# Kernel tuning notes

Hardware: AMD Instinct MI355X
Metric: run time of the kernel (lower is better)

The kernel has to match this reference:

```python
import jax, jax.numpy as jnp
import numpy as np

GROUP_SIZE = 128
N_BITS = 4
QMAX = 2 ** N_BITS - 1
NUM_EXPERTS = 8
HIDDEN = 2048
INTER = 768
NUM_ROT = 4
T_TOKENS = 4096
TOP_K = 2


def _make_pairs(rng, n_rot, in_feat):
    # intra-group permutation per rotation (valid disjoint Givens pairs)
    n_groups = in_feat // GROUP_SIZE
    return np.stack([
        np.concatenate([rng.permutation(GROUP_SIZE) for _ in range(n_groups)])
        for _ in range(n_rot)
    ]).astype(np.int32)


def _round_ste(x):
    return x + jax.lax.stop_gradient(jnp.round(x) - x)


def _rotate(W, pairs, angles):
    # W: [N, in_feat]; pairs: [R, in_feat] intra-group perm; angles: [R, in_feat//2]
    in_feat = W.shape[1]
    base = (jnp.arange(in_feat) // GROUP_SIZE) * GROUP_SIZE
    for r in range(pairs.shape[0]):
        abs_idx = base + pairs[r]
        i_idx = abs_idx[0::2]
        j_idx = abs_idx[1::2]
        c = jnp.cos(angles[r])
        s = jnp.sin(angles[r])
        wi = W[:, i_idx]
        wj = W[:, j_idx]
        W = W.at[:, i_idx].set(c * wi - s * wj).at[:, j_idx].set(s * wi + c * wj)
    return W


def _fake_quant(W):
    # groupwise asymmetric min-max fake quantization with STE rounding
    shape = W.shape
    wg = W.reshape(-1, GROUP_SIZE)
    wmax = wg.max(axis=-1, keepdims=True)
    wmin = wg.min(axis=-1, keepdims=True)
    scale = jnp.clip(wmax - wmin, 1e-5, None) / QMAX
    zero = jnp.round(-wmin / scale)
    q = jnp.clip(_round_ste(wg / scale) + zero, 0.0, float(QMAX))
    return ((q - zero) * scale).reshape(shape)


def _pseudo_quantize(W3, pairs, angles, ch_scales):
    # scale -> rotate -> fake-quant -> inverse rotate (reversed order, -angles) -> unscale
    E, O, In = W3.shape
    W = W3.reshape(-1, In) * ch_scales
    W = _rotate(W, pairs, angles)
    W = _fake_quant(W)
    W = _rotate(W, pairs[::-1], -angles[::-1])
    return (W / ch_scales).reshape(E, O, In)


def setup_inputs() -> dict:
    key = jax.random.key(0)
    ks = jax.random.split(key, 8)
    rng = np.random.default_rng(0)
    hidden_states = jax.random.normal(ks[0], (T_TOKENS, HIDDEN), jnp.float32)
    top_k_index = jax.random.randint(ks[1], (T_TOKENS, TOP_K), 0, NUM_EXPERTS, jnp.int32)
    logits = jax.random.normal(ks[2], (T_TOKENS, TOP_K), jnp.float32)
    top_k_weights = jax.nn.softmax(logits, axis=-1)
    gate_up_weight = jax.random.normal(ks[3], (NUM_EXPERTS, 2 * INTER, HIDDEN), jnp.float32) * 0.02
    down_weight = jax.random.normal(ks[4], (NUM_EXPERTS, HIDDEN, INTER), jnp.float32) * 0.02
    gate_up_pairs = jnp.asarray(_make_pairs(rng, NUM_ROT, HIDDEN))
    down_pairs = jnp.asarray(_make_pairs(rng, NUM_ROT, INTER))
    gate_up_angles = jax.random.normal(ks[5], (NUM_ROT, HIDDEN // 2), jnp.float32) * 0.1
    down_angles = jax.random.normal(ks[6], (NUM_ROT, INTER // 2), jnp.float32) * 0.1
    k7, k8 = jax.random.split(ks[7])
    gate_up_channel_scales = jax.random.uniform(k7, (1, HIDDEN), jnp.float32, 0.5, 1.5)
    down_channel_scales = jax.random.uniform(k8, (1, INTER), jnp.float32, 0.5, 1.5)
    return {
        "hidden_states": hidden_states,
        "top_k_index": top_k_index,
        "top_k_weights": top_k_weights,
        "gate_up_weight": gate_up_weight,
        "down_weight": down_weight,
        "gate_up_pairs": gate_up_pairs,
        "gate_up_angles": gate_up_angles,
        "down_pairs": down_pairs,
        "down_angles": down_angles,
        "gate_up_channel_scales": gate_up_channel_scales,
        "down_channel_scales": down_channel_scales,
    }


def reference(hidden_states, top_k_index, top_k_weights, gate_up_weight, down_weight,
              gate_up_pairs, gate_up_angles, down_pairs, down_angles,
              gate_up_channel_scales, down_channel_scales):
    # dequantize expert weights
    gup = _pseudo_quantize(gate_up_weight, gate_up_pairs, gate_up_angles, gate_up_channel_scales)  # [E,2I,H]
    dwn = _pseudo_quantize(down_weight, down_pairs, down_angles, down_channel_scales)              # [E,H,I]
    T = hidden_states.shape[0]
    E = gup.shape[0]
    # dense dispatch: all experts for all tokens (E small), combined by routing weights
    h = jnp.einsum('th,eoh->teo', hidden_states, gup)          # [T,E,2I]
    gate, up = jnp.split(h, 2, axis=-1)
    inter = jax.nn.silu(gate) * up                              # [T,E,I]
    y = jnp.einsum('tei,ehi->teh', inter, dwn)                  # [T,E,H]
    combine = jnp.zeros((T, E), hidden_states.dtype)
    combine = combine.at[jnp.arange(T)[:, None], top_k_index].add(top_k_weights)
    return jnp.einsum('teh,te->th', y, combine)
```

## Files before the change

kernel.cpp:

```cpp
#include <hip/hip_runtime.h>

#define T_TOKENS 4096
#define HIDDEN   2048
#define INTERM   768
#define NE       8
#define NPAIR    8192
#define NROT     4
#define MAXT     72

typedef __bf16 bf16x8 __attribute__((ext_vector_type(8)));
typedef float  f32x4  __attribute__((ext_vector_type(4)));

__device__ __forceinline__ unsigned short f2bf(float f) {
  unsigned u = __float_as_uint(f);
  u += 0x7fffu + ((u >> 16) & 1u);
  return (unsigned short)(u >> 16);
}

__device__ __forceinline__ void async16(const void* g, void* l) {
  __builtin_amdgcn_global_load_lds((const __attribute__((address_space(1))) void*)g,
                                   (__attribute__((address_space(3))) void*)l, 16, 0, 0);
}

__global__ void k_hist(const int* __restrict__ idx, int* __restrict__ cnt) {
  const int t = blockIdx.x * 256 + threadIdx.x;
  if (t < NPAIR) atomicAdd(&cnt[idx[t]], 1);
}

__global__ void k_scan(const int* __restrict__ cnt, int* __restrict__ off,
                       int* __restrict__ cur, int* __restrict__ tmap) {
  if (threadIdx.x == 0) {
    int a = 0, tt = 0;
    for (int e = 0; e < NE; ++e) {
      off[e] = a; cur[e] = 0;
      const int c = cnt[e];
      for (int m = 0; m < c; m += 128) tmap[tt++] = (e << 16) | (m >> 7);
      a += c;
    }
    for (; tt < MAXT; ++tt) tmap[tt] = -1;
  }
}

__global__ void k_scatter(const int* __restrict__ idx, const float* __restrict__ wts,
                          const int* __restrict__ off, int* __restrict__ cur,
                          int* __restrict__ pt, float* __restrict__ pw) {
  const int t = blockIdx.x * 256 + threadIdx.x;
  if (t < NPAIR) {
    const int e = idx[t];
    const int pos = off[e] + atomicAdd(&cur[e], 1);
    pt[pos] = t;
    pw[pos] = wts[t];
  }
}

__global__ void k_tbl(const int* __restrict__ gp, const float* __restrict__ ga,
                      const int* __restrict__ dp, const float* __restrict__ da,
                      const float* __restrict__ gch, const float* __restrict__ dch,
                      float4* __restrict__ tg, float4* __restrict__ td,
                      float* __restrict__ grch, float* __restrict__ drch) {
  const int t = blockIdx.x * 256 + threadIdx.x;
  if (t < NROT * (HIDDEN / 2)) {
    const int r = t >> 10, s = t & 1023;
    const int grp = s >> 6;
    const int i = gp[r * HIDDEN + 2 * s], j = gp[r * HIDDEN + 2 * s + 1];
    const float a = ga[r * (HIDDEN / 2) + s];
    const float c = cosf(a), sn = sinf(a);
    tg[(grp * NROT + r) * 128 + i] = make_float4(c, -sn, __int_as_float(j), 0.f);
    tg[(grp * NROT + r) * 128 + j] = make_float4(c,  sn, __int_as_float(i), 0.f);
  }
  if (t < NROT * (INTERM / 2)) {
    const int r = t / (INTERM / 2), s = t - r * (INTERM / 2);
    const int grp = s >> 6;
    const int i = dp[r * INTERM + 2 * s], j = dp[r * INTERM + 2 * s + 1];
    const float a = da[r * (INTERM / 2) + s];
    const float c = cosf(a), sn = sinf(a);
    td[(grp * NROT + r) * 128 + i] = make_float4(c, -sn, __int_as_float(j), 0.f);
    td[(grp * NROT + r) * 128 + j] = make_float4(c,  sn, __int_as_float(i), 0.f);
  }
  if (t < HIDDEN) grch[t] = 1.0f / gch[t];
  if (t < INTERM) drch[t] = 1.0f / dch[t];
}

#define FWD_ROT(tl, v0, v1)                                                     \
  _Pragma("unroll")                                                             \
  for (int r = 0; r < NROT; ++r) {                                              \
    const float4 e0 = tl[r * 128 + l];                                          \
    const float4 e1 = tl[r * 128 + 64 + l];                                     \
    const int p0 = __float_as_int(e0.z), p1 = __float_as_int(e1.z);             \
    const int a0 = (p0 & 63) << 2, a1 = (p1 & 63) << 2;                         \
    _Pragma("unroll")                                                           \
    for (int q = 0; q < 4; ++q) {                                               \
      const int x0 = __float_as_int(v0[q]), x1 = __float_as_int(v1[q]);         \
      const float lo0 = __int_as_float(__builtin_amdgcn_ds_bpermute(a0, x0));   \
      const float hi0 = __int_as_float(__builtin_amdgcn_ds_bpermute(a0, x1));   \
      const float lo1 = __int_as_float(__builtin_amdgcn_ds_bpermute(a1, x0));   \
      const float hi1 = __int_as_float(__builtin_amdgcn_ds_bpermute(a1, x1));   \
      const float op0 = (p0 & 64) ? hi0 : lo0;                                  \
      const float op1 = (p1 & 64) ? hi1 : lo1;                                  \
      {                                                                         \
        _Pragma("clang fp contract(off)")                                       \
        v0[q] = e0.x * v0[q] + e0.y * op0;                                      \
        v1[q] = e1.x * v1[q] + e1.y * op1;                                      \
      }                                                                         \
    }                                                                           \
  }

__global__ __launch_bounds__(256) void k_quant(
    const float* __restrict__ W, const float4* __restrict__ tbl,
    const float* __restrict__ ch, unsigned short* __restrict__ out, int In, int G) {
  __shared__ float4 tl[NROT * 128];
  const int wv = threadIdx.x >> 6, l = threadIdx.x & 63;
  const int g = blockIdx.x % G;
  const int rowblk = blockIdx.x / G;
  const int row0 = rowblk * 16 + wv * 4;
  const int colbase = g << 7;
  tl[threadIdx.x]       = tbl[(size_t)g * NROT * 128 + threadIdx.x];
  tl[256 + threadIdx.x] = tbl[(size_t)g * NROT * 128 + 256 + threadIdx.x];
  __syncthreads();
  const float c0 = ch[colbase + l], c1 = ch[colbase + 64 + l];
  float v0[4], v1[4];
#pragma unroll
  for (int q = 0; q < 4; ++q) {
#pragma clang fp contract(off)
    const float* Wr = W + (size_t)(row0 + q) * In + colbase;
    v0[q] = Wr[l] * c0;
    v1[q] = Wr[64 + l] * c1;
  }
  FWD_ROT(tl, v0, v1)
#pragma unroll
  for (int q = 0; q < 4; ++q) {
    float mn = fminf(v0[q], v1[q]), mx = fmaxf(v0[q], v1[q]);
#pragma unroll
    for (int o = 32; o > 0; o >>= 1) {
      mn = fminf(mn, __shfl_xor(mn, o));
      mx = fmaxf(mx, __shfl_xor(mx, o));
    }
    {
#pragma clang fp contract(off)
      const float scale = fmaxf(mx - mn, 1e-5f) / 15.0f;
      const float zero = rintf(-mn / scale);
      const float q0 = fminf(fmaxf(rintf(v0[q] / scale) + zero, 0.0f), 15.0f);
      const float q1 = fminf(fmaxf(rintf(v1[q] / scale) + zero, 0.0f), 15.0f);
      v0[q] = (q0 - zero) * scale;
      v1[q] = (q1 - zero) * scale;
    }
  }
#pragma unroll
  for (int q = 0; q < 4; ++q) {
    unsigned short* Or = out + (size_t)(row0 + q) * In + colbase;
    Or[l]      = f2bf(v0[q]);
    Or[64 + l] = f2bf(v1[q]);
  }
}

__global__ __launch_bounds__(256) void k_rotx(
    const float* __restrict__ X, const float* __restrict__ rch,
    const float4* __restrict__ tbl, unsigned short* __restrict__ out) {
  __shared__ float4 tl[NROT * 128];
  const int wv = threadIdx.x >> 6, l = threadIdx.x & 63;
  const int g = blockIdx.x % 16;
  const int rowblk = blockIdx.x / 16;
  const int row0 = rowblk * 16 + wv * 4;
  const int colbase = g << 7;
  tl[threadIdx.x]       = tbl[(size_t)g * NROT * 128 + threadIdx.x];
  tl[256 + threadIdx.x] = tbl[(size_t)g * NROT * 128 + 256 + threadIdx.x];
  __syncthreads();
  const float i0 = rch[colbase + l], i1 = rch[colbase + 64 + l];
  float v0[4], v1[4];
#pragma unroll
  for (int q = 0; q < 4; ++q) {
    const float* Xr = X + (size_t)(row0 + q) * HIDDEN + colbase;
    v0[q] = Xr[l] * i0;
    v1[q] = Xr[64 + l] * i1;
  }
  FWD_ROT(tl, v0, v1)
#pragma unroll
  for (int q = 0; q < 4; ++q) {
    unsigned short* Or = out + (size_t)(row0 + q) * HIDDEN + colbase;
    Or[l]      = f2bf(v0[q]);
    Or[64 + l] = f2bf(v1[q]);
  }
}

__global__ __launch_bounds__(256) void k_silu2(
    const float* __restrict__ h, const float* __restrict__ pw,
    const float* __restrict__ rch, const float4* __restrict__ tbl,
    unsigned short* __restrict__ out) {
  __shared__ float4 tl[NROT * 128];
  const int wv = threadIdx.x >> 6, l = threadIdx.x & 63;
  const int g = blockIdx.x % 6;
  const int rowblk = blockIdx.x / 6;
  const int row0 = rowblk * 16 + wv * 4;
  const int colbase = g << 7;
  tl[threadIdx.x]       = tbl[(size_t)g * NROT * 128 + threadIdx.x];
  tl[256 + threadIdx.x] = tbl[(size_t)g * NROT * 128 + 256 + threadIdx.x];
  __syncthreads();
  const float i0 = rch[colbase + l], i1 = rch[colbase + 64 + l];
  float v0[4], v1[4];
#pragma unroll
  for (int q = 0; q < 4; ++q) {
    const int row = row0 + q;
    const float wgt = pw[row];
    const float* hr = h + (size_t)row * 1536 + colbase;
    const float g0 = hr[l], g1 = hr[64 + l];
    const float u0 = hr[768 + l], u1 = hr[768 + 64 + l];
    v0[q] = g0 / (1.0f + expf(-g0)) * u0 * wgt * i0;
    v1[q] = g1 / (1.0f + expf(-g1)) * u1 * wgt * i1;
  }
  FWD_ROT(tl, v0, v1)
#pragma unroll
  for (int q = 0; q < 4; ++q) {
    unsigned short* Or = out + (size_t)(row0 + q) * INTERM + colbase;
    Or[l]      = f2bf(v0[q]);
    Or[64 + l] = f2bf(v1[q]);
  }
}

template <int MODE>
__launch_bounds__(256, 4)
__global__ void k_gemm(const unsigned short* __restrict__ A,
                       const unsigned short* __restrict__ Bw,
                       float* __restrict__ C,
                       const int* __restrict__ pt,
                       const int* __restrict__ off,
                       const int* __restrict__ cnt,
                       const int* __restrict__ tmap) {
  constexpr int K = MODE ? INTERM : HIDDEN;
  constexpr int N = MODE ? HIDDEN : 2 * INTERM;
  const int tm = tmap[blockIdx.y];
  if (tm < 0) return;
  const int e = tm >> 16;
  const int m0 = (tm & 0xffff) << 7;
  const int count = cnt[e];
  const int seg = off[e];
  const int n0 = blockIdx.x * 128;
  const unsigned short* Be = Bw + (size_t)e * N * K;

  __shared__ unsigned short As[2][128 * 32];
  __shared__ unsigned short Bs[2][128 * 32];

  const int tid = threadIdx.x;
  const int w = tid >> 6;
  const int l = tid & 63;
  const int r0 = w * 16 + (l >> 2);
  const int r1 = r0 + 64;
  const int kco = (l & 3) * 8;

  int p0 = m0 + r0; if (p0 > count - 1) p0 = count - 1;
  int p1 = m0 + r1; if (p1 > count - 1) p1 = count - 1;
  size_t arow0, arow1;
  if (MODE == 0) { arow0 = (size_t)(pt[seg + p0] >> 1); arow1 = (size_t)(pt[seg + p1] >> 1); }
  else           { arow0 = (size_t)(seg + p0); arow1 = (size_t)(seg + p1); }
  const unsigned short* pa0 = A + arow0 * K + kco;
  const unsigned short* pa1 = A + arow1 * K + kco;
  const unsigned short* pb0 = Be + (size_t)(n0 + r0) * K + kco;
  const unsigned short* pb1 = Be + (size_t)(n0 + r1) * K + kco;

  const int ko = (l >> 4) * 8;
  const int mrow = (w & 1) * 64 + (l & 15);
  const int nrow = (w >> 1) * 64 + (l & 15);

  f32x4 acc[4][4];
#pragma unroll
  for (int i = 0; i < 4; ++i)
#pragma unroll
    for (int j = 0; j < 4; ++j) acc[i][j] = (f32x4)0.0f;

  {
    async16(pa0, &As[0][w * 512]);
    async16(pa1, &As[0][(w + 4) * 512]);
    async16(pb0, &Bs[0][w * 512]);
    async16(pb1, &Bs[0][(w + 4) * 512]);
  }
  int buf = 0;
  for (int k0 = 0; k0 < K; k0 += 32, buf ^= 1) {
    __syncthreads();
    bf16x8 af[4], bfr[4];
#pragma unroll
    for (int i = 0; i < 4; ++i)
      af[i] = *(const bf16x8*)&As[buf][(mrow + i * 16) * 32 + ko];
#pragma unroll
    for (int j = 0; j < 4; ++j)
      bfr[j] = *(const bf16x8*)&Bs[buf][(nrow + j * 16) * 32 + ko];
    if (k0 + 32 < K) {
      const int kn = k0 + 32;
      async16(pa0 + kn, &As[buf ^ 1][w * 512]);
      async16(pa1 + kn, &As[buf ^ 1][(w + 4) * 512]);
      async16(pb0 + kn, &Bs[buf ^ 1][w * 512]);
      async16(pb1 + kn, &Bs[buf ^ 1][(w + 4) * 512]);
    }
#pragma unroll
    for (int i = 0; i < 4; ++i)
#pragma unroll
      for (int j = 0; j < 4; ++j)
        acc[i][j] = __builtin_amdgcn_mfma_f32_16x16x32_bf16(af[i], bfr[j], acc[i][j], 0, 0, 0);
  }

  const int mb = (w & 1) * 64 + (l >> 4) * 4;
  const int nb = n0 + (w >> 1) * 64 + (l & 15);
#pragma unroll
  for (int i = 0; i < 4; ++i) {
#pragma unroll
    for (int j = 0; j < 4; ++j) {
#pragma unroll
      for (int r = 0; r < 4; ++r) {
        const int mm = m0 + mb + i * 16 + r;
        if (mm < count) {
          const int nn = nb + j * 16;
          if (MODE == 0) {
            C[(size_t)(seg + mm) * N + nn] = acc[i][j][r];
          } else {
            C[(size_t)pt[seg + mm] * N + nn] = acc[i][j][r];
          }
        }
      }
    }
  }
}

__global__ __launch_bounds__(256) void k_combine(const float4* __restrict__ y,
                                                 float4* __restrict__ out) {
  const int t = blockIdx.x;
  const float4* y0 = y + (size_t)(2 * t) * (HIDDEN / 4);
  const float4* y1 = y + (size_t)(2 * t + 1) * (HIDDEN / 4);
  float4* o = out + (size_t)t * (HIDDEN / 4);
#pragma unroll
  for (int q = 0; q < 2; ++q) {
    const int c = threadIdx.x + q * 256;
    const float4 a = y0[c], b = y1[c];
    o[c] = make_float4(a.x + b.x, a.y + b.y, a.z + b.z, a.w + b.w);
  }
}

extern "C" void kernel_launch(void* const* d_in, const int* in_sizes, int n_in,
                              void* d_out, int out_size, void* d_ws, size_t ws_size,
                              hipStream_t stream) {
  const float* hs  = (const float*)d_in[0];
  const int*   tki = (const int*)d_in[1];
  const float* tkw = (const float*)d_in[2];
  const float* guw = (const float*)d_in[3];
  const float* dww = (const float*)d_in[4];
  const int*   gupr= (const int*)d_in[5];
  const float* gua = (const float*)d_in[6];
  const int*   dwp = (const int*)d_in[7];
  const float* dwa = (const float*)d_in[8];
  const float* gus = (const float*)d_in[9];
  const float* dwsc= (const float*)d_in[10];
  float* out = (float*)d_out;
  char* ws = (char*)d_ws;

  unsigned short* gup_bf = (unsigned short*)(ws + 0);
  unsigned short* dwn_bf = (unsigned short*)(ws + 50331648);
  unsigned short* x_bf   = (unsigned short*)(ws + 75497472);
  float*          hbuf   = (float*)(ws + 92274688);
  unsigned short* interb = (unsigned short*)(ws + 142606336);
  float*          ybuf   = (float*)(ws + 75497472);
  int*            pt     = (int*)(ws + 155189248);
  float*          pw     = (float*)(ws + 155222016);
  int*            cnt    = (int*)(ws + 155254784);
  int*            off    = cnt + 8;
  int*            cur    = cnt + 16;
  int*            tmap   = cnt + 24;
  float4*         tg     = (float4*)(ws + 155258880);
  float4*         td     = (float4*)(ws + 155389952);
  float*          grch   = (float*)(ws + 155439104);
  float*          drch   = (float*)(ws + 155447296);

  (void)hipMemsetAsync(cnt, 0, 32, stream);

  k_hist<<<32, 256, 0, stream>>>(tki, cnt);
  k_scan<<<1, 64, 0, stream>>>(cnt, off, cur, tmap);
  k_scatter<<<32, 256, 0, stream>>>(tki, tkw, off, cur, pt, pw);
  k_tbl<<<16, 256, 0, stream>>>(gupr, gua, dwp, dwa, gus, dwsc, tg, td, grch, drch);
  k_rotx<<<4096, 256, 0, stream>>>(hs, grch, tg, x_bf);
  k_quant<<<12288, 256, 0, stream>>>(guw, tg, gus, gup_bf, HIDDEN, 16);
  k_quant<<<6144, 256, 0, stream>>>(dww, td, dwsc, dwn_bf, INTERM, 6);
  k_gemm<0><<<dim3(12, MAXT), 256, 0, stream>>>(x_bf, gup_bf, hbuf, pt, off, cnt, tmap);
  k_silu2<<<3072, 256, 0, stream>>>(hbuf, pw, drch, td, interb);
  k_gemm<1><<<dim3(16, MAXT), 256, 0, stream>>>(interb, dwn_bf, ybuf, pt, off, cnt, tmap);
  k_combine<<<T_TOKENS, 256, 0, stream>>>((const float4*)ybuf, (float4*)out);
}
```

Before: 543.2 us.

## Remap GEMM blocks per XCD for L2 locality and reorder LDS loads after prefetch

```diff
diff --git a/kernel.cpp b/kernel.cpp
--- a/kernel.cpp
+++ b/kernel.cpp
@@ -28,7 +28,8 @@
 }
 
 __global__ void k_scan(const int* __restrict__ cnt, int* __restrict__ off,
-                       int* __restrict__ cur, int* __restrict__ tmap) {
+                       int* __restrict__ cur, int* __restrict__ tmap,
+                       int* __restrict__ nv) {
   if (threadIdx.x == 0) {
     int a = 0, tt = 0;
     for (int e = 0; e < NE; ++e) {
@@ -37,6 +38,7 @@
       for (int m = 0; m < c; m += 128) tmap[tt++] = (e << 16) | (m >> 7);
       a += c;
     }
+    nv[0] = tt;
     for (; tt < MAXT; ++tt) tmap[tt] = -1;
   }
 }
@@ -224,16 +226,37 @@
                        const int* __restrict__ pt,
                        const int* __restrict__ off,
                        const int* __restrict__ cnt,
-                       const int* __restrict__ tmap) {
+                       const int* __restrict__ tmap,
+                       const int* __restrict__ nv) {
   constexpr int K = MODE ? INTERM : HIDDEN;
   constexpr int N = MODE ? HIDDEN : 2 * INTERM;
-  const int tm = tmap[blockIdx.y];
+  constexpr int XW = MODE ? 16 : 12;
+
+  const int hw  = blockIdx.x + XW * blockIdx.y;
+  const int xcd = hw & 7;
+  const int pos = hw >> 3;
+  const int nvalid = nv[0];
+  const int q8 = nvalid >> 3, r8 = nvalid & 7;
+  const int rs = q8 + (xcd < r8 ? 1 : 0);
+  const int y0 = xcd * q8 + (xcd < r8 ? xcd : r8);
+  if (pos >= rs * XW) return;
+  int xg, yg;
+  if (MODE == 1) {
+    xg = pos & 15; yg = y0 + (pos >> 4);
+  } else {
+    const int cap6 = rs * 6;
+    const int half = (pos >= cap6) ? 1 : 0;
+    const int rem  = pos - half * cap6;
+    xg = half * 6 + rem % 6;
+    yg = y0 + rem / 6;
+  }
+  const int tm = tmap[yg];
   if (tm < 0) return;
   const int e = tm >> 16;
   const int m0 = (tm & 0xffff) << 7;
   const int count = cnt[e];
   const int seg = off[e];
-  const int n0 = blockIdx.x * 128;
+  const int n0 = xg * 128;
   const unsigned short* Be = Bw + (size_t)e * N * K;
 
   __shared__ unsigned short As[2][128 * 32];
@@ -275,13 +298,6 @@
   int buf = 0;
   for (int k0 = 0; k0 < K; k0 += 32, buf ^= 1) {
     __syncthreads();
-    bf16x8 af[4], bfr[4];
-#pragma unroll
-    for (int i = 0; i < 4; ++i)
-      af[i] = *(const bf16x8*)&As[buf][(mrow + i * 16) * 32 + ko];
-#pragma unroll
-    for (int j = 0; j < 4; ++j)
-      bfr[j] = *(const bf16x8*)&Bs[buf][(nrow + j * 16) * 32 + ko];
     if (k0 + 32 < K) {
       const int kn = k0 + 32;
       async16(pa0 + kn, &As[buf ^ 1][w * 512]);
@@ -289,6 +305,13 @@
       async16(pb0 + kn, &Bs[buf ^ 1][w * 512]);
       async16(pb1 + kn, &Bs[buf ^ 1][(w + 4) * 512]);
     }
+    bf16x8 af[4], bfr[4];
+#pragma unroll
+    for (int i = 0; i < 4; ++i)
+      af[i] = *(const bf16x8*)&As[buf][(mrow + i * 16) * 32 + ko];
+#pragma unroll
+    for (int j = 0; j < 4; ++j)
+      bfr[j] = *(const bf16x8*)&Bs[buf][(nrow + j * 16) * 32 + ko];
 #pragma unroll
     for (int i = 0; i < 4; ++i)
 #pragma unroll
@@ -361,6 +384,7 @@
   int*            off    = cnt + 8;
   int*            cur    = cnt + 16;
   int*            tmap   = cnt + 24;
+  int*            nv     = cnt + 120;
   float4*         tg     = (float4*)(ws + 155258880);
   float4*         td     = (float4*)(ws + 155389952);
   float*          grch   = (float*)(ws + 155439104);
@@ -369,14 +393,14 @@
   (void)hipMemsetAsync(cnt, 0, 32, stream);
 
   k_hist<<<32, 256, 0, stream>>>(tki, cnt);
-  k_scan<<<1, 64, 0, stream>>>(cnt, off, cur, tmap);
+  k_scan<<<1, 64, 0, stream>>>(cnt, off, cur, tmap, nv);
   k_scatter<<<32, 256, 0, stream>>>(tki, tkw, off, cur, pt, pw);
   k_tbl<<<16, 256, 0, stream>>>(gupr, gua, dwp, dwa, gus, dwsc, tg, td, grch, drch);
   k_rotx<<<4096, 256, 0, stream>>>(hs, grch, tg, x_bf);
   k_quant<<<12288, 256, 0, stream>>>(guw, tg, gus, gup_bf, HIDDEN, 16);
   k_quant<<<6144, 256, 0, stream>>>(dww, td, dwsc, dwn_bf, INTERM, 6);
-  k_gemm<0><<<dim3(12, MAXT), 256, 0, stream>>>(x_bf, gup_bf, hbuf, pt, off, cnt, tmap);
+  k_gemm<0><<<dim3(12, MAXT), 256, 0, stream>>>(x_bf, gup_bf, hbuf, pt, off, cnt, tmap, nv);
   k_silu2<<<3072, 256, 0, stream>>>(hbuf, pw, drch, td, interb);
-  k_gemm<1><<<dim3(16, MAXT), 256, 0, stream>>>(interb, dwn_bf, ybuf, pt, off, cnt, tmap);
+  k_gemm<1><<<dim3(16, MAXT), 256, 0, stream>>>(interb, dwn_bf, ybuf, pt, off, cnt, tmap, nv);
   k_combine<<<T_TOKENS, 256, 0, stream>>>((const float4*)ybuf, (float4*)out);
 }
```

Measured after the change: 536.3 us. No clear change (-1.3%).
